# Kernel tuning notes

Hardware: AMD Instinct MI355X
Metric: run time of the kernel (lower is better)

## Reference

```python
import jax, jax.numpy as jnp
import numpy as np

M, N, K = 1024, 11008, 4096


def _unpack_i2u(Bp):
    """Unpack 2-bit unsigned weights per decode_i2u_to_i8s interleave.

    Bp: [N, K//4] int8 storage. Within each group of 4 bytes (16 elements),
    output element at position 4*i + j = (byte_j >> (2*i)) & 3.
    Returns [N, K] int8 with values in {0,1,2,3}.
    """
    Bu = jax.lax.bitcast_convert_type(Bp, jnp.uint8)  # [N, K//4]
    n, kc = Bu.shape
    Bg = Bu.reshape(n, kc // 4, 1, 4)                 # [N, G, 1, j]
    shifts = (jnp.arange(4, dtype=jnp.uint8) * jnp.uint8(2)).reshape(1, 1, 4, 1)
    vals = (Bg >> shifts) & jnp.uint8(3)              # [N, G, i, j]
    return vals.reshape(n, kc * 4).astype(jnp.int8)   # [N, K]


def setup_inputs() -> dict:
    key = jax.random.key(0)
    k1, k2 = jax.random.split(key)
    A = jax.random.randint(k1, (M, K), -128, 128, dtype=jnp.int8)
    B = jax.random.randint(k2, (N, K // 4), -128, 128, dtype=jnp.int8)
    return {"A": A, "B": B}


def reference(A, B):
    W = _unpack_i2u(B)  # [N, K] int8
    C = jax.lax.dot_general(
        A, W,
        dimension_numbers=(((1,), (1,)), ((), ())),
        preferred_element_type=jnp.int32,
    )  # [M, N] int32
    return C
```

## Files before the change

kernel.cpp:

```cpp
#include <hip/hip_runtime.h>
#include <stdint.h>


#define MM 1024
#define NN 11008
#define KK 4096
#define KSTEPS (KK / 64)

using i32x4  = __attribute__((ext_vector_type(4))) int;
using i32x16 = __attribute__((ext_vector_type(16))) int;

__device__ __forceinline__ int pack4(i32x4 v) {
    return (int)(((uint32_t)v[0] & 0xFFu) | (((uint32_t)v[1] & 0xFFu) << 8)
               | (((uint32_t)v[2] & 0xFFu) << 16) | (((uint32_t)v[3] & 0xFFu) << 24));
}

__global__ __launch_bounds__(256) void prep_A(const int* __restrict__ src,
                                              uint8_t* __restrict__ dst) {
    const int t = blockIdx.x * 256 + threadIdx.x;
    const int m = t >> 8, k16 = t & 255;
    const i32x4* s4 = (const i32x4*)(src + (((size_t)m << 8) + k16) * 16);
    i32x4 o;
#pragma unroll
    for (int q = 0; q < 4; ++q) o[q] = pack4(s4[q]);
    const int kstep = k16 >> 2;
    const int chunk = (k16 & 3) ^ (m & 3);
    *(i32x4*)(dst + (size_t)kstep * (MM * 64) + m * 64 + chunk * 16) = o;
}

__global__ __launch_bounds__(256) void prep_B(const int* __restrict__ src,
                                              uint8_t* __restrict__ dst) {
    const int t = blockIdx.x * 256 + threadIdx.x;
    const int n = t >> 6, kg = t & 63;
    const i32x4* s4 = (const i32x4*)(src + (((size_t)n << 6) + kg) * 16);
    int w[4];
#pragma unroll
    for (int d = 0; d < 4; ++d) w[d] = pack4(s4[d]);
    const int x = (n >> 3) & 1;
    i32x4 o;
    o[0] = x ? w[1] : w[0];
    o[1] = x ? w[0] : w[1];
    o[2] = x ? w[3] : w[2];
    o[3] = x ? w[2] : w[3];
    *(i32x4*)(dst + (size_t)kg * (NN * 16) + n * 16) = o;
}

#define GLOAD_LDS16(g, l) __builtin_amdgcn_global_load_lds(                    \
        (const __attribute__((address_space(1))) uint32_t*)(g),                \
        (__attribute__((address_space(3))) uint32_t*)(l), 16, 0, 0)

__global__ __launch_bounds__(256) void bitnet_gemm(const uint8_t* __restrict__ A2,
                                                   const uint8_t* __restrict__ B2,
                                                   int* __restrict__ C) {
    const int t    = threadIdx.x;
    const int lane = t & 63, wave = t >> 6;
    const int wr   = wave >> 1, wc = wave & 1;
    const int l31  = lane & 31, h = lane >> 5;
    const int brow = blockIdx.y * 128, bcol = blockIdx.x * 128;

    __shared__ __align__(16) uint8_t As[2][8192];
    __shared__ __align__(16) uint8_t Bs[2][2048];

    int a_off[2][2], b_off[2][2];
#pragma unroll
    for (int mi = 0; mi < 2; ++mi)
#pragma unroll
        for (int kk2 = 0; kk2 < 2; ++kk2) {
            const int row   = wr * 64 + mi * 32 + l31;
            const int chunk = (kk2 * 2 + h) ^ (row & 3);
            a_off[mi][kk2]  = row * 64 + chunk * 16;
        }
#pragma unroll
    for (int ni = 0; ni < 2; ++ni)
#pragma unroll
        for (int kk2 = 0; kk2 < 2; ++kk2) {
            const int n   = wc * 64 + ni * 32 + l31;
            const int d   = kk2 * 2 + (h ^ ((n >> 3) & 1));
            b_off[ni][kk2] = n * 16 + d * 4;
        }

    const uint8_t* gA = A2 + (size_t)brow * 64 + t * 16;
    const uint8_t* gB = B2 + (size_t)bcol * 16 + t * 16;

    i32x16 acc[2][2] = {};

    auto STAGE = [&](int buf, int ks) {
        const uint8_t* at = gA + (size_t)ks * (MM * 64);
        GLOAD_LDS16(at,        &As[buf][wave * 1024]);
        GLOAD_LDS16(at + 4096, &As[buf][4096 + wave * 1024]);
        if (wave < 2) {
            const uint8_t* bt = gB + (size_t)ks * (NN * 16);
            GLOAD_LDS16(bt, &Bs[buf][wave * 1024]);
        }
    };

    auto COMPUTE = [&](int buf) {
        const uint8_t* ab = As[buf];
        const uint8_t* bb = Bs[buf];
#pragma unroll
        for (int kk2 = 0; kk2 < 2; ++kk2) {
            i32x4 a0 = *(const i32x4*)(ab + a_off[0][kk2]);
            i32x4 a1 = *(const i32x4*)(ab + a_off[1][kk2]);
            const uint32_t p0 = *(const uint32_t*)(bb + b_off[0][kk2]);
            const uint32_t p1 = *(const uint32_t*)(bb + b_off[1][kk2]);
            i32x4 b0, b1;
#pragma unroll
            for (int i = 0; i < 4; ++i) {
                b0[i] = (int)((p0 >> (2 * i)) & 0x03030303u);
                b1[i] = (int)((p1 >> (2 * i)) & 0x03030303u);
            }
            acc[0][0] = __builtin_amdgcn_mfma_i32_32x32x32_i8(a0, b0, acc[0][0], 0, 0, 0);
            acc[0][1] = __builtin_amdgcn_mfma_i32_32x32x32_i8(a0, b1, acc[0][1], 0, 0, 0);
            acc[1][0] = __builtin_amdgcn_mfma_i32_32x32x32_i8(a1, b0, acc[1][0], 0, 0, 0);
            acc[1][1] = __builtin_amdgcn_mfma_i32_32x32x32_i8(a1, b1, acc[1][1], 0, 0, 0);
        }
    };

    STAGE(0, 0);
    __syncthreads();

#pragma unroll 1
    for (int ks = 0; ks < KSTEPS - 2; ks += 2) {
        STAGE(1, ks + 1);
        COMPUTE(0);
        __syncthreads();
        STAGE(0, ks + 2);
        COMPUTE(1);
        __syncthreads();
    }
    STAGE(1, KSTEPS - 1);
    COMPUTE(0);
    __syncthreads();
    COMPUTE(1);

#pragma unroll
    for (int mi = 0; mi < 2; ++mi)
#pragma unroll
        for (int ni = 0; ni < 2; ++ni) {
            const int colg = bcol + wc * 64 + ni * 32 + l31;
#pragma unroll
            for (int r = 0; r < 16; ++r) {
                const int rowin = (r & 3) + 8 * (r >> 2) + 4 * h;
                const int rowg  = brow + wr * 64 + mi * 32 + rowin;
                C[(size_t)rowg * NN + colg] = acc[mi][ni][r];
            }
        }
}

extern "C" void kernel_launch(void* const* d_in, const int* in_sizes, int n_in,
                              void* d_out, int out_size, void* d_ws, size_t ws_size,
                              hipStream_t stream) {
    const int* A32 = (const int*)d_in[0];
    const int* B32 = (const int*)d_in[1];
    int* C = (int*)d_out;

    uint8_t* A2 = (uint8_t*)d_ws;
    uint8_t* B2 = A2 + (size_t)MM * KK;

    prep_A<<<dim3((MM * KK / 16) / 256), dim3(256), 0, stream>>>(A32, A2);
    prep_B<<<dim3((NN * 64) / 256), dim3(256), 0, stream>>>(B32, B2);
    bitnet_gemm<<<dim3(NN / 128, MM / 128), dim3(256), 0, stream>>>(A2, B2, C);
}
```

Baseline: 72.55 us.

## Pre-tile A and B into per-block fragment order for contiguous staging

The prep kernels now write A and B in a tile-major layout: each (kstep, tile) block is a contiguous chunk already ordered by wave, fragment and lane. The GEMM stages each tile with fully contiguous global-to-LDS loads and reads fragments at simple lane-linear LDS offsets, replacing the XOR-swizzled offset tables. This is meant to improve global load coalescing and LDS access patterns. In exchange, the prep kernels' reads become more scattered, and the linear lane-major LDS reads may hit different bank patterns.

```diff
diff --git a/kernel.cpp b/kernel.cpp
--- a/kernel.cpp
+++ b/kernel.cpp
@@ -6,6 +6,8 @@
 #define NN 11008
 #define KK 4096
 #define KSTEPS (KK / 64)
+#define MTILES (MM / 128)
+#define NTILES (NN / 128)
 
 using i32x4  = __attribute__((ext_vector_type(4))) int;
 using i32x16 = __attribute__((ext_vector_type(16))) int;
@@ -17,32 +19,40 @@
 
 __global__ __launch_bounds__(256) void prep_A(const int* __restrict__ src,
                                               uint8_t* __restrict__ dst) {
-    const int t = blockIdx.x * 256 + threadIdx.x;
-    const int m = t >> 8, k16 = t & 255;
-    const i32x4* s4 = (const i32x4*)(src + (((size_t)m << 8) + k16) * 16);
+    const int g = blockIdx.x * 256 + threadIdx.x;
+    const int kstep = g >> 12;
+    const int rem   = g & 4095;
+    const int mtile = rem >> 9;
+    const int c     = rem & 511;
+    const int wr  = (c >> 8) & 1, mi = (c >> 7) & 1, kk2 = (c >> 6) & 1;
+    const int lane = c & 63;
+    const int row   = mtile * 128 + wr * 64 + mi * 32 + (lane & 31);
+    const int kbyte = kstep * 64 + kk2 * 32 + (lane >> 5) * 16;
+    const i32x4* s4 = (const i32x4*)(src + (size_t)row * KK + kbyte);
     i32x4 o;
 #pragma unroll
     for (int q = 0; q < 4; ++q) o[q] = pack4(s4[q]);
-    const int kstep = k16 >> 2;
-    const int chunk = (k16 & 3) ^ (m & 3);
-    *(i32x4*)(dst + (size_t)kstep * (MM * 64) + m * 64 + chunk * 16) = o;
+    *(i32x4*)(dst + (size_t)g * 16) = o;
 }
 
 __global__ __launch_bounds__(256) void prep_B(const int* __restrict__ src,
                                               uint8_t* __restrict__ dst) {
     const int t = blockIdx.x * 256 + threadIdx.x;
-    const int n = t >> 6, kg = t & 63;
-    const i32x4* s4 = (const i32x4*)(src + (((size_t)n << 6) + kg) * 16);
-    int w[4];
+    const int kstep = t / (NTILES * 128);
+    const int rem   = t % (NTILES * 128);
+    const int ntile = rem >> 7;
+    const int c     = rem & 127;
+    const int d0    = c * 4;
+    const int wc  = (d0 >> 8) & 1, ni = (d0 >> 7) & 1, kk2 = (d0 >> 6) & 1;
+    const int j   = kk2 * 2 + ((d0 & 63) >> 5);
+    const int n0  = ntile * 128 + wc * 64 + ni * 32 + (d0 & 31);
+    i32x4 o;
 #pragma unroll
-    for (int d = 0; d < 4; ++d) w[d] = pack4(s4[d]);
-    const int x = (n >> 3) & 1;
-    i32x4 o;
-    o[0] = x ? w[1] : w[0];
-    o[1] = x ? w[0] : w[1];
-    o[2] = x ? w[3] : w[2];
-    o[3] = x ? w[2] : w[3];
-    *(i32x4*)(dst + (size_t)kg * (NN * 16) + n * 16) = o;
+    for (int q = 0; q < 4; ++q) {
+        const i32x4 v = *(const i32x4*)(src + (size_t)(n0 + q) * (KK / 4) + kstep * 16 + j * 4);
+        o[q] = pack4(v);
+    }
+    *(i32x4*)(dst + (size_t)t * 16) = o;
 }
 
 #define GLOAD_LDS16(g, l) __builtin_amdgcn_global_load_lds(                    \
@@ -56,41 +66,20 @@
     const int lane = t & 63, wave = t >> 6;
     const int wr   = wave >> 1, wc = wave & 1;
     const int l31  = lane & 31, h = lane >> 5;
-    const int brow = blockIdx.y * 128, bcol = blockIdx.x * 128;
+    const int by   = blockIdx.y, bx = blockIdx.x;
 
     __shared__ __align__(16) uint8_t As[2][8192];
     __shared__ __align__(16) uint8_t Bs[2][2048];
 
-    int a_off[2][2], b_off[2][2];
-#pragma unroll
-    for (int mi = 0; mi < 2; ++mi)
-#pragma unroll
-        for (int kk2 = 0; kk2 < 2; ++kk2) {
-            const int row   = wr * 64 + mi * 32 + l31;
-            const int chunk = (kk2 * 2 + h) ^ (row & 3);
-            a_off[mi][kk2]  = row * 64 + chunk * 16;
-        }
-#pragma unroll
-    for (int ni = 0; ni < 2; ++ni)
-#pragma unroll
-        for (int kk2 = 0; kk2 < 2; ++kk2) {
-            const int n   = wc * 64 + ni * 32 + l31;
-            const int d   = kk2 * 2 + (h ^ ((n >> 3) & 1));
-            b_off[ni][kk2] = n * 16 + d * 4;
-        }
-
-    const uint8_t* gA = A2 + (size_t)brow * 64 + t * 16;
-    const uint8_t* gB = B2 + (size_t)bcol * 16 + t * 16;
-
     i32x16 acc[2][2] = {};
 
     auto STAGE = [&](int buf, int ks) {
-        const uint8_t* at = gA + (size_t)ks * (MM * 64);
-        GLOAD_LDS16(at,        &As[buf][wave * 1024]);
-        GLOAD_LDS16(at + 4096, &As[buf][4096 + wave * 1024]);
+        const uint8_t* at = A2 + ((size_t)ks * MTILES + by) * 8192;
+        GLOAD_LDS16(at + t * 16,        &As[buf][wave * 1024]);
+        GLOAD_LDS16(at + 4096 + t * 16, &As[buf][4096 + wave * 1024]);
         if (wave < 2) {
-            const uint8_t* bt = gB + (size_t)ks * (NN * 16);
-            GLOAD_LDS16(bt, &Bs[buf][wave * 1024]);
+            const uint8_t* bt = B2 + ((size_t)ks * NTILES + bx) * 2048;
+            GLOAD_LDS16(bt + t * 16, &Bs[buf][wave * 1024]);
         }
     };
 
@@ -99,10 +88,10 @@
         const uint8_t* bb = Bs[buf];
 #pragma unroll
         for (int kk2 = 0; kk2 < 2; ++kk2) {
-            i32x4 a0 = *(const i32x4*)(ab + a_off[0][kk2]);
-            i32x4 a1 = *(const i32x4*)(ab + a_off[1][kk2]);
-            const uint32_t p0 = *(const uint32_t*)(bb + b_off[0][kk2]);
-            const uint32_t p1 = *(const uint32_t*)(bb + b_off[1][kk2]);
+            i32x4 a0 = *(const i32x4*)(ab + ((wr * 2 + 0) * 2 + kk2) * 1024 + lane * 16);
+            i32x4 a1 = *(const i32x4*)(ab + ((wr * 2 + 1) * 2 + kk2) * 1024 + lane * 16);
+            const uint32_t p0 = *(const uint32_t*)(bb + ((wc * 2 + 0) * 2 + kk2) * 256 + lane * 4);
+            const uint32_t p1 = *(const uint32_t*)(bb + ((wc * 2 + 1) * 2 + kk2) * 256 + lane * 4);
             i32x4 b0, b1;
 #pragma unroll
             for (int i = 0; i < 4; ++i) {
@@ -133,6 +122,7 @@
     __syncthreads();
     COMPUTE(1);
 
+    const int brow = by * 128, bcol = bx * 128;
 #pragma unroll
     for (int mi = 0; mi < 2; ++mi)
 #pragma unroll
@@ -159,5 +149,5 @@
 
     prep_A<<<dim3((MM * KK / 16) / 256), dim3(256), 0, stream>>>(A32, A2);
     prep_B<<<dim3((NN * 64) / 256), dim3(256), 0, stream>>>(B32, B2);
-    bitnet_gemm<<<dim3(NN / 128, MM / 128), dim3(256), 0, stream>>>(A2, B2, C);
+    bitnet_gemm<<<dim3(NTILES, MTILES), dim3(256), 0, stream>>>(A2, B2, C);
 }
```

Result: slower. 75.96 us (+4.7%).
